# Performance work log

Hardware: AMD Instinct MI355X
Metric: run time of the kernel (lower is better)

Reference implementation:

```python
import jax, jax.numpy as jnp
import numpy as np

N, E, IN = 90000, 540000, 30
H1, H2, H3, H4 = 128, 128, 128, 64

def _glorot(k, i, o):
    return jax.random.normal(k, (i, o), jnp.float32) * np.float32(np.sqrt(2.0 / (i + o)))

def setup_inputs() -> dict:
    key = jax.random.key(0)
    ks = jax.random.split(key, 20)
    inp = {
        'x': jax.random.normal(ks[0], (N, IN), jnp.float32),
        'edge_index': jax.random.randint(ks[1], (2, E), 0, N, dtype=jnp.int32),
    }
    shapes = [(IN, H1), (H1, H2), (H2, H3), (H3, H4)]
    i = 2
    for br in ('s', 't'):
        for li, (din, dout) in enumerate(shapes, start=1):
            inp[f'w{li}{br}'] = _glorot(ks[i], din, dout); i += 1
            inp[f'b{li}{br}'] = jnp.zeros((dout,), jnp.float32)
    return inp

def _mlp(h, w1, b1, w2, b2):
    # Linear -> (Dropout eval = identity) -> ReLU -> Linear
    return jax.nn.relu(h @ w1 + b1) @ w2 + b2

def _gin(h, src, dst, w1, b1, w2, b2):
    # GINConv with eps=0: MLP(x_i + sum_{j->i} x_j)
    agg = jax.ops.segment_sum(h[src], dst, num_segments=N)
    return _mlp(h + agg, w1, b1, w2, b2)

def reference(x, edge_index, w1s, b1s, w2s, b2s, w3s, b3s, w4s, b4s,
              w1t, b1t, w2t, b2t, w3t, b3t, w4t, b4t):
    src, dst = edge_index[0], edge_index[1]
    z_src = _gin(x, src, dst, w1s, b1s, w2s, b2s)       # [N, H2]
    z_src = _gin(z_src, src, dst, w3s, b3s, w4s, b4s)   # [N, H4]
    z_tar = _gin(x, src, dst, w1t, b1t, w2t, b2t)
    z_tar = _gin(z_tar, src, dst, w3t, b3t, w4t, b4t)
    zs = z_src.reshape(-1, 9, H4)  # [G, 9, H4]
    zt = z_tar.reshape(-1, 9, H4)
    adj = jnp.einsum('gik,gjk->gij', zs, zt)  # per-graph 9x9 matmul
    return adj.reshape(-1, 9)  # [N, 9], matches torch.cat along dim 0
```

## Files before the change

kernel.cpp:

```cpp
#include <hip/hip_runtime.h>
#include <hip/hip_bf16.h>


typedef __attribute__((ext_vector_type(8))) short short8;
typedef __attribute__((ext_vector_type(4))) float f32x4;

#define MAXDEG 64

__device__ inline unsigned short f2bf(float f) {
    union { float f; unsigned u; } v; v.f = f;
    unsigned r = v.u + 0x7fffu + ((v.u >> 16) & 1u);
    return (unsigned short)(r >> 16);
}
__device__ inline float bflo(unsigned u) { return __uint_as_float(u << 16); }
__device__ inline float bfhi(unsigned u) { return __uint_as_float(u & 0xffff0000u); }
__device__ inline unsigned packbf(float a, float b) {
    return (unsigned)f2bf(a) | ((unsigned)f2bf(b) << 16);
}

#define W1S_OFF 0
#define W2S_OFF 4096
#define W3S_OFF 20480
#define W4S_OFF 36864
#define W1T_OFF 45056
#define W2T_OFF 49152
#define W3T_OFF 65536
#define W4T_OFF 81920
#define PACK_USHORTS 90112

__global__ __launch_bounds__(64) void wpack_kernel(
    const float* w0, const float* w1, const float* w2, const float* w3,
    const float* w4, const float* w5, const float* w6, const float* w7,
    unsigned short* __restrict__ pack)
{
    const int prefix[9] = {0, 8, 40, 72, 88, 96, 128, 160, 176};
    const int KTa[8] = {1, 4, 4, 4, 1, 4, 4, 4};
    const int KRa[8] = {30, 128, 128, 128, 30, 128, 128, 128};
    const int Ca[8]  = {128, 128, 128, 64, 128, 128, 128, 64};
    const int DOFF[8] = {W1S_OFF, W2S_OFF, W3S_OFF, W4S_OFF,
                         W1T_OFF, W2T_OFF, W3T_OFF, W4T_OFF};
    const float* Ws[8] = {w0, w1, w2, w3, w4, w5, w6, w7};
    int bid = blockIdx.x;
    int mi = 0;
    while (mi < 7 && bid >= prefix[mi + 1]) ++mi;
    int lt = bid - prefix[mi];
    int kt = lt % KTa[mi], ct = lt / KTa[mi];
    const float* W = Ws[mi];
    int l = threadIdx.x;
    int n = ct * 16 + (l & 15);
    for (int j = 0; j < 8; ++j) {
        int k = kt * 32 + (l >> 4) * 8 + j;
        float v = (k < KRa[mi]) ? W[(size_t)k * Ca[mi] + n] : 0.f;
        pack[(size_t)DOFF[mi] + (size_t)lt * 512 + l * 8 + j] = f2bf(v);
    }
}

__global__ __launch_bounds__(256) void xpad_zero_kernel(
    const float* __restrict__ x, float* __restrict__ xpad,
    int* __restrict__ deg, int N)
{
    int gid = blockIdx.x * 256 + threadIdx.x;
    if (gid < N) deg[gid] = 0;
    if (gid >= N * 32) return;
    int n = gid >> 5, f = gid & 31;
    xpad[gid] = (f < 30) ? x[(size_t)n * 30 + f] : 0.f;
}

__global__ __launch_bounds__(256) void bucket_kernel(
    const int* __restrict__ src, const int* __restrict__ dst,
    int* __restrict__ deg, int* __restrict__ colb, int E)
{
    int e = blockIdx.x * 256 + threadIdx.x;
    if (e < E) {
        int d = dst[e];
        int slot = atomicAdd(&deg[d], 1);
        if (slot < MAXDEG) colb[(size_t)d * MAXDEG + slot] = src[e];
    }
}

__global__ __launch_bounds__(256) void gather30_kernel(
    const float* __restrict__ xpad, const int* __restrict__ deg,
    const int* __restrict__ colb, unsigned short* __restrict__ h1, int N)
{
    int gid = blockIdx.x * 256 + threadIdx.x;
    int node = gid >> 3;
    if (node >= N) return;
    int l = gid & 7;
    const float4* base = (const float4*)xpad;
    float4 a = base[(size_t)node * 8 + l];
    const int* col = colb + (size_t)node * MAXDEG;
    int e = min(deg[node], MAXDEG);
    int i = 0;
    for (; i + 4 <= e; i += 4) {
        int s0 = col[i], s1 = col[i + 1], s2 = col[i + 2], s3 = col[i + 3];
        float4 v0 = base[(size_t)s0 * 8 + l];
        float4 v1 = base[(size_t)s1 * 8 + l];
        float4 v2 = base[(size_t)s2 * 8 + l];
        float4 v3 = base[(size_t)s3 * 8 + l];
        a.x += v0.x; a.y += v0.y; a.z += v0.z; a.w += v0.w;
        a.x += v1.x; a.y += v1.y; a.z += v1.z; a.w += v1.w;
        a.x += v2.x; a.y += v2.y; a.z += v2.z; a.w += v2.w;
        a.x += v3.x; a.y += v3.y; a.z += v3.z; a.w += v3.w;
    }
    for (; i + 2 <= e; i += 2) {
        int s0 = col[i], s1 = col[i + 1];
        float4 v0 = base[(size_t)s0 * 8 + l];
        float4 v1 = base[(size_t)s1 * 8 + l];
        a.x += v0.x; a.y += v0.y; a.z += v0.z; a.w += v0.w;
        a.x += v1.x; a.y += v1.y; a.z += v1.z; a.w += v1.w;
    }
    for (; i < e; ++i) {
        float4 v0 = base[(size_t)col[i] * 8 + l];
        a.x += v0.x; a.y += v0.y; a.z += v0.z; a.w += v0.w;
    }
    uint2 o; o.x = packbf(a.x, a.y); o.y = packbf(a.z, a.w);
    ((uint2*)h1)[(size_t)node * 8 + l] = o;
}

__global__ __launch_bounds__(256) void mlp1_kernel(
    const unsigned short* __restrict__ h1, const unsigned short* __restrict__ pack,
    const float* __restrict__ b1s, const float* __restrict__ b2s,
    const float* __restrict__ b1t, const float* __restrict__ b2t,
    unsigned short* __restrict__ z1cat, int N)
{
    __shared__ __align__(16) unsigned short hs[64 * 40];
    __shared__ __align__(16) unsigned short hm[64 * 136];
    const int tid = threadIdx.x;
    const int n0blk = blockIdx.x * 64;

    {
        int row = tid >> 2, off = tid & 3;
        int gn = n0blk + row;
        short8 v = {0, 0, 0, 0, 0, 0, 0, 0};
        if (gn < N) v = *(const short8*)&h1[(size_t)gn * 32 + off * 8];
        *(short8*)&hs[row * 40 + off * 8] = v;
    }
    __syncthreads();

    const int wv = tid >> 6, l = tid & 63, q = l >> 4, m = l & 15;

    for (int br = 0; br < 2; ++br) {
        const float* B1 = br ? b1t : b1s;
        const float* B2 = br ? b2t : b2s;
        const int w1off = br ? W1T_OFF : W1S_OFF;
        const int w2off = br ? W2T_OFF : W2S_OFF;

        {
            short8 a[4];
            #pragma unroll
            for (int nt = 0; nt < 4; ++nt)
                a[nt] = *(const short8*)&hs[(nt * 16 + m) * 40 + q * 8];
            #pragma unroll
            for (int ci = 0; ci < 2; ++ci) {
                int ct = wv * 2 + ci;
                short8 bf = *(const short8*)&pack[w1off + ((size_t)ct * 64 + l) * 8];
                float bias = B1[ct * 16 + m];
                #pragma unroll
                for (int nt = 0; nt < 4; ++nt) {
                    f32x4 acc = {0.f, 0.f, 0.f, 0.f};
                    acc = __builtin_amdgcn_mfma_f32_16x16x32_bf16(a[nt], bf, acc, 0, 0, 0);
                    #pragma unroll
                    for (int r = 0; r < 4; ++r) {
                        float v = fmaxf(acc[r] + bias, 0.f);
                        hm[(nt * 16 + q * 4 + r) * 136 + ct * 16 + m] = f2bf(v);
                    }
                }
            }
        }
        __syncthreads();

        f32x4 acc2[4][2];
        #pragma unroll
        for (int nt = 0; nt < 4; ++nt)
            #pragma unroll
            for (int ci = 0; ci < 2; ++ci)
                acc2[nt][ci] = (f32x4){0.f, 0.f, 0.f, 0.f};
        for (int nt = 0; nt < 4; ++nt) {
            short8 a[4];
            #pragma unroll
            for (int kt = 0; kt < 4; ++kt)
                a[kt] = *(const short8*)&hm[(nt * 16 + m) * 136 + kt * 32 + q * 8];
            #pragma unroll
            for (int ci = 0; ci < 2; ++ci) {
                int ct = wv * 2 + ci;
                #pragma unroll
                for (int kt = 0; kt < 4; ++kt) {
                    short8 bf = *(const short8*)&pack[w2off + ((size_t)(ct * 4 + kt) * 64 + l) * 8];
                    acc2[nt][ci] = __builtin_amdgcn_mfma_f32_16x16x32_bf16(a[kt], bf, acc2[nt][ci], 0, 0, 0);
                }
            }
        }
        __syncthreads();
        #pragma unroll
        for (int ci = 0; ci < 2; ++ci) {
            int ct = wv * 2 + ci;
            float bias = B2[ct * 16 + m];
            #pragma unroll
            for (int nt = 0; nt < 4; ++nt)
                #pragma unroll
                for (int r = 0; r < 4; ++r)
                    hm[(nt * 16 + q * 4 + r) * 136 + ct * 16 + m] =
                        f2bf(acc2[nt][ci][r] + bias);
        }
        __syncthreads();
        for (int c = tid; c < 1024; c += 256) {
            int row = c >> 4, off = c & 15;
            int gn = n0blk + row;
            if (gn < N) {
                short8 v = *(const short8*)&hm[row * 136 + off * 8];
                *(short8*)&z1cat[(size_t)gn * 256 + br * 128 + off * 8] = v;
            }
        }
        __syncthreads();
    }
}

__global__ __launch_bounds__(512, 8) void mlp2_kernel(
    const unsigned short* __restrict__ z1, const int* __restrict__ deg,
    const int* __restrict__ colb, const unsigned short* __restrict__ pack,
    const float* __restrict__ b3s, const float* __restrict__ b4s,
    const float* __restrict__ b3t, const float* __restrict__ b4t,
    float* __restrict__ z2cat, int N)
{
    __shared__ __align__(16) unsigned short hs[32 * 264];
    __shared__ __align__(16) unsigned short hm[32 * 136];
    const int tid = threadIdx.x;
    const int n0blk = blockIdx.x * 32;

    {
        const int g = tid >> 5, l = tid & 31;
        const uint4* base = (const uint4*)z1;
        for (int it = 0; it < 2; ++it) {
            int row = it * 16 + g;
            int gn = n0blk + row;
            float a0 = 0.f, a1 = 0.f, a2 = 0.f, a3 = 0.f;
            float a4 = 0.f, a5 = 0.f, a6 = 0.f, a7 = 0.f;
            if (gn < N) {
                uint4 s = base[(size_t)gn * 32 + l];
                a0 = bflo(s.x); a1 = bfhi(s.x); a2 = bflo(s.y); a3 = bfhi(s.y);
                a4 = bflo(s.z); a5 = bfhi(s.z); a6 = bflo(s.w); a7 = bfhi(s.w);
                const int* col = colb + (size_t)gn * MAXDEG;
                int e = min(deg[gn], MAXDEG);
                int i = 0;
                for (; i + 4 <= e; i += 4) {
                    int s0 = col[i], s1 = col[i + 1], s2 = col[i + 2], s3 = col[i + 3];
                    uint4 v0 = base[(size_t)s0 * 32 + l];
                    uint4 v1 = base[(size_t)s1 * 32 + l];
                    uint4 v2 = base[(size_t)s2 * 32 + l];
                    uint4 v3 = base[(size_t)s3 * 32 + l];
                    a0 += bflo(v0.x); a1 += bfhi(v0.x); a2 += bflo(v0.y); a3 += bfhi(v0.y);
                    a4 += bflo(v0.z); a5 += bfhi(v0.z); a6 += bflo(v0.w); a7 += bfhi(v0.w);
                    a0 += bflo(v1.x); a1 += bfhi(v1.x); a2 += bflo(v1.y); a3 += bfhi(v1.y);
                    a4 += bflo(v1.z); a5 += bfhi(v1.z); a6 += bflo(v1.w); a7 += bfhi(v1.w);
                    a0 += bflo(v2.x); a1 += bfhi(v2.x); a2 += bflo(v2.y); a3 += bfhi(v2.y);
                    a4 += bflo(v2.z); a5 += bfhi(v2.z); a6 += bflo(v2.w); a7 += bfhi(v2.w);
                    a0 += bflo(v3.x); a1 += bfhi(v3.x); a2 += bflo(v3.y); a3 += bfhi(v3.y);
                    a4 += bflo(v3.z); a5 += bfhi(v3.z); a6 += bflo(v3.w); a7 += bfhi(v3.w);
                }
                for (; i + 2 <= e; i += 2) {
                    int s0 = col[i], s1 = col[i + 1];
                    uint4 v0 = base[(size_t)s0 * 32 + l];
                    uint4 v1 = base[(size_t)s1 * 32 + l];
                    a0 += bflo(v0.x); a1 += bfhi(v0.x); a2 += bflo(v0.y); a3 += bfhi(v0.y);
                    a4 += bflo(v0.z); a5 += bfhi(v0.z); a6 += bflo(v0.w); a7 += bfhi(v0.w);
                    a0 += bflo(v1.x); a1 += bfhi(v1.x); a2 += bflo(v1.y); a3 += bfhi(v1.y);
                    a4 += bflo(v1.z); a5 += bfhi(v1.z); a6 += bflo(v1.w); a7 += bfhi(v1.w);
                }
                for (; i < e; ++i) {
                    uint4 v0 = base[(size_t)col[i] * 32 + l];
                    a0 += bflo(v0.x); a1 += bfhi(v0.x); a2 += bflo(v0.y); a3 += bfhi(v0.y);
                    a4 += bflo(v0.z); a5 += bfhi(v0.z); a6 += bflo(v0.w); a7 += bfhi(v0.w);
                }
            }
            short8 st;
            st[0] = (short)f2bf(a0); st[1] = (short)f2bf(a1);
            st[2] = (short)f2bf(a2); st[3] = (short)f2bf(a3);
            st[4] = (short)f2bf(a4); st[5] = (short)f2bf(a5);
            st[6] = (short)f2bf(a6); st[7] = (short)f2bf(a7);
            *(short8*)&hs[row * 264 + l * 8] = st;
        }
    }
    __syncthreads();

    const int wv = tid >> 6, l = tid & 63, q = l >> 4, m = l & 15;

    for (int br = 0; br < 2; ++br) {
        const int w1off = br ? W3T_OFF : W3S_OFF;
        const int w2off = br ? W4T_OFF : W4S_OFF;
        const float* B1 = br ? b3t : b3s;
        const float* B2 = br ? b4t : b4s;
        if (br) __syncthreads();

        #pragma unroll
        for (int ti = 0; ti < 2; ++ti) {
            const int tile = wv * 2 + ti;
            const int ct = tile & 7;
            const int nt = tile >> 3;
            float bias = B1[ct * 16 + m];
            short8 a[4];
            #pragma unroll
            for (int kt = 0; kt < 4; ++kt)
                a[kt] = *(const short8*)&hs[(nt * 16 + m) * 264 + br * 128 + kt * 32 + q * 8];
            f32x4 acc = {0.f, 0.f, 0.f, 0.f};
            #pragma unroll
            for (int kt = 0; kt < 4; ++kt) {
                short8 bf = *(const short8*)&pack[w1off + ((size_t)(ct * 4 + kt) * 64 + l) * 8];
                acc = __builtin_amdgcn_mfma_f32_16x16x32_bf16(a[kt], bf, acc, 0, 0, 0);
            }
            #pragma unroll
            for (int r = 0; r < 4; ++r) {
                float v = fmaxf(acc[r] + bias, 0.f);
                hm[(nt * 16 + q * 4 + r) * 136 + ct * 16 + m] = f2bf(v);
            }
        }
        __syncthreads();

        {
            const int ct = wv & 3;
            const int nt = wv >> 2;
            float bias = B2[ct * 16 + m];
            short8 a[4];
            #pragma unroll
            for (int kt = 0; kt < 4; ++kt)
                a[kt] = *(const short8*)&hm[(nt * 16 + m) * 136 + kt * 32 + q * 8];
            f32x4 acc = {0.f, 0.f, 0.f, 0.f};
            #pragma unroll
            for (int kt = 0; kt < 4; ++kt) {
                short8 bf = *(const short8*)&pack[w2off + ((size_t)(ct * 4 + kt) * 64 + l) * 8];
                acc = __builtin_amdgcn_mfma_f32_16x16x32_bf16(a[kt], bf, acc, 0, 0, 0);
            }
            #pragma unroll
            for (int r = 0; r < 4; ++r) {
                int gn = n0blk + nt * 16 + q * 4 + r;
                if (gn < N)
                    z2cat[(size_t)gn * 128 + br * 64 + ct * 16 + m] = acc[r] + bias;
            }
        }
    }
}

__global__ __launch_bounds__(256) void einsum9_kernel(
    const float* __restrict__ z2cat, float* __restrict__ out, int G)
{
    int g0 = blockIdx.x * 3;
    __shared__ float ss[27][68];
    __shared__ float tt[27][68];
    const int tid = threadIdx.x;
    for (int idx = tid; idx < 27 * 16; idx += 256) {
        int n = idx >> 4, k4 = idx & 15;
        int g = g0 + n / 9;
        if (g < G) {
            size_t row = (size_t)(g * 9 + (n % 9)) * 128;
            float4 a = *(const float4*)&z2cat[row + k4 * 4];
            float4 b = *(const float4*)&z2cat[row + 64 + k4 * 4];
            *(float4*)&ss[n][k4 * 4] = a;
            *(float4*)&tt[n][k4 * 4] = b;
        }
    }
    __syncthreads();
    if (tid < 243) {
        int gl = tid / 81, rem = tid - gl * 81;
        int i = rem / 9, j = rem - i * 9;
        int g = g0 + gl;
        if (g < G) {
            float acc = 0.f;
            #pragma unroll
            for (int k = 0; k < 64; ++k) acc += ss[gl * 9 + i][k] * tt[gl * 9 + j][k];
            out[(size_t)g * 81 + i * 9 + j] = acc;
        }
    }
}

extern "C" void kernel_launch(void* const* d_in, const int* in_sizes, int n_in,
                              void* d_out, int out_size, void* d_ws, size_t ws_size,
                              hipStream_t stream)
{
    const float* x  = (const float*)d_in[0];
    const int*   ei = (const int*)d_in[1];
    const int N_ = in_sizes[0] / 30;
    const int E_ = in_sizes[1] / 2;
    const int* src = ei;
    const int* dst = ei + E_;

    const float* w1s = (const float*)d_in[2];
    const float* b1s = (const float*)d_in[3];
    const float* w2s = (const float*)d_in[4];
    const float* b2s = (const float*)d_in[5];
    const float* w3s = (const float*)d_in[6];
    const float* b3s = (const float*)d_in[7];
    const float* w4s = (const float*)d_in[8];
    const float* b4s = (const float*)d_in[9];
    const float* w1t = (const float*)d_in[10];
    const float* b1t = (const float*)d_in[11];
    const float* w2t = (const float*)d_in[12];
    const float* b2t = (const float*)d_in[13];
    const float* w3t = (const float*)d_in[14];
    const float* b3t = (const float*)d_in[15];
    const float* w4t = (const float*)d_in[16];
    const float* b4t = (const float*)d_in[17];

    int* deg  = (int*)d_ws;
    int* colb = deg + N_;
    size_t int_bytes = ((size_t)N_ * (1 + MAXDEG)) * sizeof(int);
    size_t pb = (int_bytes + 15) & ~(size_t)15;
    unsigned short* packu = (unsigned short*)((char*)d_ws + pb);
    float* xpad = (float*)(packu + PACK_USHORTS);
    unsigned short* h1    = (unsigned short*)(xpad + (size_t)N_ * 32);
    unsigned short* z1cat = h1 + (size_t)N_ * 32;
    float* z2cat = (float*)(z1cat + (size_t)N_ * 256);
    size_t need = pb + (size_t)PACK_USHORTS * 2
                + (size_t)N_ * 32 * 4
                + (size_t)N_ * 32 * 2
                + (size_t)N_ * 256 * 2
                + (size_t)N_ * 128 * 4;
    if (ws_size < need) return;

    const int nbE  = (E_ + 255) / 256;
    const int nb64 = (N_ + 63) / 64;
    const int nb32 = (N_ + 31) / 32;

    wpack_kernel<<<176, 64, 0, stream>>>(w1s, w2s, w3s, w4s,
                                         w1t, w2t, w3t, w4t, packu);
    xpad_zero_kernel<<<(N_ * 32 + 255) / 256, 256, 0, stream>>>(x, xpad, deg, N_);

    bucket_kernel<<<nbE, 256, 0, stream>>>(src, dst, deg, colb, E_);

    gather30_kernel<<<(N_ * 8 + 255) / 256, 256, 0, stream>>>(
        xpad, deg, colb, h1, N_);

    mlp1_kernel<<<nb64, 256, 0, stream>>>(h1, packu,
        b1s, b2s, b1t, b2t, z1cat, N_);

    mlp2_kernel<<<nb32, 512, 0, stream>>>(z1cat, deg, colb, packu,
        b3s, b4s, b3t, b4t, z2cat, N_);

    {
        int G = N_ / 9;
        einsum9_kernel<<<(G + 2) / 3, 256, 0, stream>>>(z2cat, (float*)d_out, G);
    }
}
```

Before: 247.0 us.

## Merge prep kernels, run both MLP1 branches concurrently, widen einsum blocks

Fuses the weight-pack and xpad/degree-zero kernels into one launch to save a kernel launch. Splits mlp1 into two 256-thread halves that compute the s and t branches in parallel with separate shared buffers, and writes the second-layer outputs straight to global instead of staging them through shared memory. This removes several block-wide barriers but produces scattered 2-byte global stores. The einsum kernel now handles 6 graphs per 512-thread block instead of 3 per 256-thread block.

```diff
diff --git a/kernel.cpp b/kernel.cpp
--- a/kernel.cpp
+++ b/kernel.cpp
@@ -27,43 +27,44 @@
 #define W3T_OFF 65536
 #define W4T_OFF 81920
 #define PACK_USHORTS 90112
-
-__global__ __launch_bounds__(64) void wpack_kernel(
+#define WPACK_BLOCKS 176
+
+__global__ __launch_bounds__(256) void prep_kernel(
     const float* w0, const float* w1, const float* w2, const float* w3,
     const float* w4, const float* w5, const float* w6, const float* w7,
-    unsigned short* __restrict__ pack)
-{
-    const int prefix[9] = {0, 8, 40, 72, 88, 96, 128, 160, 176};
-    const int KTa[8] = {1, 4, 4, 4, 1, 4, 4, 4};
-    const int KRa[8] = {30, 128, 128, 128, 30, 128, 128, 128};
-    const int Ca[8]  = {128, 128, 128, 64, 128, 128, 128, 64};
-    const int DOFF[8] = {W1S_OFF, W2S_OFF, W3S_OFF, W4S_OFF,
-                         W1T_OFF, W2T_OFF, W3T_OFF, W4T_OFF};
-    const float* Ws[8] = {w0, w1, w2, w3, w4, w5, w6, w7};
-    int bid = blockIdx.x;
-    int mi = 0;
-    while (mi < 7 && bid >= prefix[mi + 1]) ++mi;
-    int lt = bid - prefix[mi];
-    int kt = lt % KTa[mi], ct = lt / KTa[mi];
-    const float* W = Ws[mi];
-    int l = threadIdx.x;
-    int n = ct * 16 + (l & 15);
-    for (int j = 0; j < 8; ++j) {
-        int k = kt * 32 + (l >> 4) * 8 + j;
-        float v = (k < KRa[mi]) ? W[(size_t)k * Ca[mi] + n] : 0.f;
-        pack[(size_t)DOFF[mi] + (size_t)lt * 512 + l * 8 + j] = f2bf(v);
-    }
-}
-
-__global__ __launch_bounds__(256) void xpad_zero_kernel(
+    unsigned short* __restrict__ pack,
     const float* __restrict__ x, float* __restrict__ xpad,
     int* __restrict__ deg, int N)
 {
-    int gid = blockIdx.x * 256 + threadIdx.x;
-    if (gid < N) deg[gid] = 0;
-    if (gid >= N * 32) return;
-    int n = gid >> 5, f = gid & 31;
-    xpad[gid] = (f < 30) ? x[(size_t)n * 30 + f] : 0.f;
+    if (blockIdx.x < WPACK_BLOCKS) {
+        if (threadIdx.x >= 64) return;
+        const int prefix[9] = {0, 8, 40, 72, 88, 96, 128, 160, 176};
+        const int KTa[8] = {1, 4, 4, 4, 1, 4, 4, 4};
+        const int KRa[8] = {30, 128, 128, 128, 30, 128, 128, 128};
+        const int Ca[8]  = {128, 128, 128, 64, 128, 128, 128, 64};
+        const int DOFF[8] = {W1S_OFF, W2S_OFF, W3S_OFF, W4S_OFF,
+                             W1T_OFF, W2T_OFF, W3T_OFF, W4T_OFF};
+        const float* Ws[8] = {w0, w1, w2, w3, w4, w5, w6, w7};
+        int bid = blockIdx.x;
+        int mi = 0;
+        while (mi < 7 && bid >= prefix[mi + 1]) ++mi;
+        int lt = bid - prefix[mi];
+        int kt = lt % KTa[mi], ct = lt / KTa[mi];
+        const float* W = Ws[mi];
+        int l = threadIdx.x;
+        int n = ct * 16 + (l & 15);
+        for (int j = 0; j < 8; ++j) {
+            int k = kt * 32 + (l >> 4) * 8 + j;
+            float v = (k < KRa[mi]) ? W[(size_t)k * Ca[mi] + n] : 0.f;
+            pack[(size_t)DOFF[mi] + (size_t)lt * 512 + l * 8 + j] = f2bf(v);
+        }
+    } else {
+        int gid = (blockIdx.x - WPACK_BLOCKS) * 256 + threadIdx.x;
+        if (gid < N) deg[gid] = 0;
+        if (gid >= N * 32) return;
+        int n = gid >> 5, f = gid & 31;
+        xpad[gid] = (f < 30) ? x[(size_t)n * 30 + f] : 0.f;
+    }
 }
 
 __global__ __launch_bounds__(256) void bucket_kernel(
@@ -117,101 +118,82 @@
     ((uint2*)h1)[(size_t)node * 8 + l] = o;
 }
 
-__global__ __launch_bounds__(256) void mlp1_kernel(
+__global__ __launch_bounds__(512, 8) void mlp1_kernel(
     const unsigned short* __restrict__ h1, const unsigned short* __restrict__ pack,
     const float* __restrict__ b1s, const float* __restrict__ b2s,
     const float* __restrict__ b1t, const float* __restrict__ b2t,
     unsigned short* __restrict__ z1cat, int N)
 {
     __shared__ __align__(16) unsigned short hs[64 * 40];
-    __shared__ __align__(16) unsigned short hm[64 * 136];
+    __shared__ __align__(16) unsigned short hm[2][64 * 136];
     const int tid = threadIdx.x;
     const int n0blk = blockIdx.x * 64;
 
     {
-        int row = tid >> 2, off = tid & 3;
+        int row = tid >> 3, off = tid & 7;
         int gn = n0blk + row;
-        short8 v = {0, 0, 0, 0, 0, 0, 0, 0};
-        if (gn < N) v = *(const short8*)&h1[(size_t)gn * 32 + off * 8];
-        *(short8*)&hs[row * 40 + off * 8] = v;
+        uint2 v = {0u, 0u};
+        if (gn < N) v = *(const uint2*)&h1[(size_t)gn * 32 + off * 4];
+        *(uint2*)&hs[row * 40 + off * 4] = v;
     }
     __syncthreads();
 
-    const int wv = tid >> 6, l = tid & 63, q = l >> 4, m = l & 15;
-
-    for (int br = 0; br < 2; ++br) {
-        const float* B1 = br ? b1t : b1s;
-        const float* B2 = br ? b2t : b2s;
-        const int w1off = br ? W1T_OFF : W1S_OFF;
-        const int w2off = br ? W2T_OFF : W2S_OFF;
-
-        {
-            short8 a[4];
-            #pragma unroll
-            for (int nt = 0; nt < 4; ++nt)
-                a[nt] = *(const short8*)&hs[(nt * 16 + m) * 40 + q * 8];
-            #pragma unroll
-            for (int ci = 0; ci < 2; ++ci) {
-                int ct = wv * 2 + ci;
-                short8 bf = *(const short8*)&pack[w1off + ((size_t)ct * 64 + l) * 8];
-                float bias = B1[ct * 16 + m];
-                #pragma unroll
-                for (int nt = 0; nt < 4; ++nt) {
-                    f32x4 acc = {0.f, 0.f, 0.f, 0.f};
-                    acc = __builtin_amdgcn_mfma_f32_16x16x32_bf16(a[nt], bf, acc, 0, 0, 0);
-                    #pragma unroll
-                    for (int r = 0; r < 4; ++r) {
-                        float v = fmaxf(acc[r] + bias, 0.f);
-                        hm[(nt * 16 + q * 4 + r) * 136 + ct * 16 + m] = f2bf(v);
-                    }
-                }
-            }
-        }
-        __syncthreads();
-
-        f32x4 acc2[4][2];
+    const int half = tid >> 8;
+    const int ltid = tid & 255;
+    const int wv = ltid >> 6, l = ltid & 63, q = l >> 4, m = l & 15;
+    const float* B1 = half ? b1t : b1s;
+    const float* B2 = half ? b2t : b2s;
+    const int w1off = half ? W1T_OFF : W1S_OFF;
+    const int w2off = half ? W2T_OFF : W2S_OFF;
+    unsigned short* hmb = hm[half];
+
+    {
+        short8 a[4];
         #pragma unroll
         for (int nt = 0; nt < 4; ++nt)
-            #pragma unroll
-            for (int ci = 0; ci < 2; ++ci)
-                acc2[nt][ci] = (f32x4){0.f, 0.f, 0.f, 0.f};
-        for (int nt = 0; nt < 4; ++nt) {
-            short8 a[4];
-            #pragma unroll
-            for (int kt = 0; kt < 4; ++kt)
-                a[kt] = *(const short8*)&hm[(nt * 16 + m) * 136 + kt * 32 + q * 8];
-            #pragma unroll
-            for (int ci = 0; ci < 2; ++ci) {
-                int ct = wv * 2 + ci;
-                #pragma unroll
-                for (int kt = 0; kt < 4; ++kt) {
-                    short8 bf = *(const short8*)&pack[w2off + ((size_t)(ct * 4 + kt) * 64 + l) * 8];
-                    acc2[nt][ci] = __builtin_amdgcn_mfma_f32_16x16x32_bf16(a[kt], bf, acc2[nt][ci], 0, 0, 0);
-                }
-            }
-        }
-        __syncthreads();
+            a[nt] = *(const short8*)&hs[(nt * 16 + m) * 40 + q * 8];
         #pragma unroll
         for (int ci = 0; ci < 2; ++ci) {
             int ct = wv * 2 + ci;
+            short8 bf = *(const short8*)&pack[w1off + ((size_t)ct * 64 + l) * 8];
+            float bias = B1[ct * 16 + m];
+            #pragma unroll
+            for (int nt = 0; nt < 4; ++nt) {
+                f32x4 acc = {0.f, 0.f, 0.f, 0.f};
+                acc = __builtin_amdgcn_mfma_f32_16x16x32_bf16(a[nt], bf, acc, 0, 0, 0);
+                #pragma unroll
+                for (int r = 0; r < 4; ++r) {
+                    float v = fmaxf(acc[r] + bias, 0.f);
+                    hmb[(nt * 16 + q * 4 + r) * 136 + ct * 16 + m] = f2bf(v);
+                }
+            }
+        }
+    }
+    __syncthreads();
+
+    for (int nt = 0; nt < 4; ++nt) {
+        short8 a[4];
+        #pragma unroll
+        for (int kt = 0; kt < 4; ++kt)
+            a[kt] = *(const short8*)&hmb[(nt * 16 + m) * 136 + kt * 32 + q * 8];
+        #pragma unroll
+        for (int ci = 0; ci < 2; ++ci) {
+            int ct = wv * 2 + ci;
+            f32x4 acc = {0.f, 0.f, 0.f, 0.f};
+            #pragma unroll
+            for (int kt = 0; kt < 4; ++kt) {
+                short8 bf = *(const short8*)&pack[w2off + ((size_t)(ct * 4 + kt) * 64 + l) * 8];
+                acc = __builtin_amdgcn_mfma_f32_16x16x32_bf16(a[kt], bf, acc, 0, 0, 0);
+            }
             float bias = B2[ct * 16 + m];
             #pragma unroll
-            for (int nt = 0; nt < 4; ++nt)
-                #pragma unroll
-                for (int r = 0; r < 4; ++r)
-                    hm[(nt * 16 + q * 4 + r) * 136 + ct * 16 + m] =
-                        f2bf(acc2[nt][ci][r] + bias);
-        }
-        __syncthreads();
-        for (int c = tid; c < 1024; c += 256) {
-            int row = c >> 4, off = c & 15;
-            int gn = n0blk + row;
-            if (gn < N) {
-                short8 v = *(const short8*)&hm[row * 136 + off * 8];
-                *(short8*)&z1cat[(size_t)gn * 256 + br * 128 + off * 8] = v;
-            }
-        }
-        __syncthreads();
+            for (int r = 0; r < 4; ++r) {
+                int gn = n0blk + nt * 16 + q * 4 + r;
+                if (gn < N)
+                    z1cat[(size_t)gn * 256 + half * 128 + ct * 16 + m] =
+                        f2bf(acc[r] + bias);
+            }
+        }
     }
 }
 
@@ -339,14 +321,14 @@
     }
 }
 
-__global__ __launch_bounds__(256) void einsum9_kernel(
+__global__ __launch_bounds__(512) void einsum9_kernel(
     const float* __restrict__ z2cat, float* __restrict__ out, int G)
 {
-    int g0 = blockIdx.x * 3;
-    __shared__ float ss[27][68];
-    __shared__ float tt[27][68];
+    int g0 = blockIdx.x * 6;
+    __shared__ float ss[54][68];
+    __shared__ float tt[54][68];
     const int tid = threadIdx.x;
-    for (int idx = tid; idx < 27 * 16; idx += 256) {
+    for (int idx = tid; idx < 54 * 16; idx += 512) {
         int n = idx >> 4, k4 = idx & 15;
         int g = g0 + n / 9;
         if (g < G) {
@@ -358,7 +340,7 @@
         }
     }
     __syncthreads();
-    if (tid < 243) {
+    if (tid < 486) {
         int gl = tid / 81, rem = tid - gl * 81;
         int i = rem / 9, j = rem - i * 9;
         int g = g0 + gl;
@@ -419,16 +401,15 @@
     const int nb64 = (N_ + 63) / 64;
     const int nb32 = (N_ + 31) / 32;
 
-    wpack_kernel<<<176, 64, 0, stream>>>(w1s, w2s, w3s, w4s,
-                                         w1t, w2t, w3t, w4t, packu);
-    xpad_zero_kernel<<<(N_ * 32 + 255) / 256, 256, 0, stream>>>(x, xpad, deg, N_);
+    prep_kernel<<<WPACK_BLOCKS + (N_ * 32 + 255) / 256, 256, 0, stream>>>(
+        w1s, w2s, w3s, w4s, w1t, w2t, w3t, w4t, packu, x, xpad, deg, N_);
 
     bucket_kernel<<<nbE, 256, 0, stream>>>(src, dst, deg, colb, E_);
 
     gather30_kernel<<<(N_ * 8 + 255) / 256, 256, 0, stream>>>(
         xpad, deg, colb, h1, N_);
 
-    mlp1_kernel<<<nb64, 256, 0, stream>>>(h1, packu,
+    mlp1_kernel<<<nb64, 512, 0, stream>>>(h1, packu,
         b1s, b2s, b1t, b2t, z1cat, N_);
 
     mlp2_kernel<<<nb32, 512, 0, stream>>>(z1cat, deg, colb, packu,
@@ -436,6 +417,6 @@
 
     {
         int G = N_ / 9;
-        einsum9_kernel<<<(G + 2) / 3, 256, 0, stream>>>(z2cat, (float*)d_out, G);
-    }
-}
+        einsum9_kernel<<<(G + 5) / 6, 512, 0, stream>>>(z2cat, (float*)d_out, G);
+    }
+}
```

Result: slower. 271.5 us (+9.9%).
